# Kernel optimization log

Measured on AMD Instinct MI355X. Metric: run time of the kernel, lower is better.

Reference implementation:

```python
import jax, jax.numpy as jnp
import numpy as np

N_NODES = 100000
N_EDGES = 600000
DIM = 128


def mish(v):
    return v * jnp.tanh(jax.nn.softplus(v))


def setup_inputs() -> dict:
    key = jax.random.key(0)
    ks = jax.random.split(key, 10)
    x = jax.random.normal(ks[0], (N_NODES, DIM), dtype=jnp.float32)
    edge_attr = jax.random.normal(ks[1], (N_EDGES, DIM), dtype=jnp.float32)
    # build edges with src < dst guaranteed (so the torch mask edge_index[0]<edge_index[1] is all True)
    a = jax.random.randint(ks[2], (N_EDGES,), 0, N_NODES - 1)
    b = jax.random.randint(ks[3], (N_EDGES,), 0, N_NODES - 1)
    src = jnp.minimum(a, b)
    dst = jnp.maximum(a, b) + (src == jnp.maximum(a, b)).astype(a.dtype)  # fix ties, stays < N_NODES
    edge_index = jnp.stack([src, dst]).astype(jnp.int64)
    s1 = 1.0 / np.sqrt(2 * DIM)
    s2 = 1.0 / np.sqrt(DIM)
    eW1 = jax.random.uniform(ks[4], (2 * DIM, DIM), jnp.float32, -s1, s1)
    eW2 = jax.random.uniform(ks[5], (DIM, DIM), jnp.float32, -s2, s2)
    nW1 = jax.random.uniform(ks[6], (2 * DIM, DIM), jnp.float32, -s1, s1)
    nW2 = jax.random.uniform(ks[7], (DIM, DIM), jnp.float32, -s2, s2)
    zb = jnp.zeros((DIM,), jnp.float32)
    return {"x": x, "edge_attr": edge_attr, "edge_index": edge_index,
            "eW1": eW1, "eb1": zb, "eW2": eW2, "eb2": zb,
            "nW1": nW1, "nb1": zb, "nW2": nW2, "nb2": zb}


def reference(x, edge_attr, edge_index, eW1, eb1, eW2, eb2, nW1, nb1, nW2, nb2):
    src, dst = edge_index[0], edge_index[1]
    # mask src < dst is all-True by construction of edge_index (see setup_inputs)
    e_in = jnp.concatenate([edge_attr, x[src] + x[dst]], axis=-1)      # [E, 2d]
    e = mish(e_in @ eW1 + eb1) @ eW2 + eb2                             # [E, d]
    agg = jax.ops.segment_sum(edge_attr, dst, num_segments=N_NODES)    # scatter_sum over dst, padded to N
    x_in = jnp.concatenate([x, agg], axis=-1)                          # [N, 2d]
    x_out = mish(x_in @ nW1 + nb1) @ nW2 + nb2                         # [N, d]
    return x_out, e
```

## Files before the change

### kernel.cpp

```cpp
#include <hip/hip_runtime.h>

#define N_NODES 100000
#define N_EDGES 600000
#define DIM 128

#define AGG_BLOCKS  1024
#define EDGE_BLOCKS 2048

typedef __attribute__((ext_vector_type(8))) short short8;
typedef __attribute__((ext_vector_type(4))) float floatx4;
typedef unsigned short ushort_t;

#define MFMA(a,b,c) __builtin_amdgcn_mfma_f32_16x16x32_bf16((a),(b),(c),0,0,0)

__device__ __forceinline__ void bar_sync() {
    asm volatile("s_waitcnt lgkmcnt(0)" ::: "memory");
    __builtin_amdgcn_s_barrier();
    asm volatile("" ::: "memory");
}

__device__ __forceinline__ unsigned short f2bf(float f) {
    unsigned int u = __float_as_uint(f);
    u += 0x7fffu + ((u >> 16) & 1u);
    return (unsigned short)(u >> 16);
}

__device__ __forceinline__ short8 pack8(const float4& a, const float4& b) {
    short8 r;
    r[0] = (short)f2bf(a.x); r[1] = (short)f2bf(a.y);
    r[2] = (short)f2bf(a.z); r[3] = (short)f2bf(a.w);
    r[4] = (short)f2bf(b.x); r[5] = (short)f2bf(b.y);
    r[6] = (short)f2bf(b.z); r[7] = (short)f2bf(b.w);
    return r;
}

__device__ __forceinline__ short8 addpack_bf(short8 a, short8 b) {
    short8 r;
    #pragma unroll
    for (int i = 0; i < 8; ++i) {
        const float fa = __uint_as_float(((unsigned int)(unsigned short)a[i]) << 16);
        const float fb = __uint_as_float(((unsigned int)(unsigned short)b[i]) << 16);
        r[i] = (short)f2bf(fa + fb);
    }
    return r;
}

__device__ __forceinline__ float mish_f(float v) {
    if (v > 30.0f) return v;
    float t = __expf(v);
    float z = 1.0f + t;
    float z2 = z * z;
    return v * (z2 - 1.0f) / (z2 + 1.0f);
}

__device__ __forceinline__ short8 load_bfrag(const float* __restrict__ W,
                                             int ct, int kt, int lane) {
    const float* p = W + (size_t)(kt * 32 + (lane >> 4) * 8) * DIM + ct * 16 + (lane & 15);
    short8 r;
    #pragma unroll
    for (int j = 0; j < 8; ++j) r[j] = (short)f2bf(p[(size_t)j * DIM]);
    return r;
}

__device__ __forceinline__ void mlp_core(
    const ushort_t* __restrict__ s_in, ushort_t* __restrict__ s_h,
    const short8 (&w1f)[8], const short8 (&w2f)[4],
    float b1v, float b2v, float* __restrict__ out, int wave, int lane)
{
    const int r0 = lane & 15, q = lane >> 4, sw = lane & 7;

    floatx4 acc0 = {0.f,0.f,0.f,0.f}, acc1 = acc0;
    #pragma unroll
    for (int kt = 0; kt < 8; ++kt) {
        const int g = kt * 4 + q;
        short8 a0 = *(const short8*)&s_in[r0 * 256 + (g ^ sw) * 8];
        short8 a1 = *(const short8*)&s_in[(16 + r0) * 256 + (g ^ sw) * 8];
        acc0 = MFMA(a0, w1f[kt], acc0);
        acc1 = MFMA(a1, w1f[kt], acc1);
    }

    const int colg = wave * 2 + (r0 >> 3);
    const int bq   = r0 & 7;
    #pragma unroll
    for (int i = 0; i < 4; ++i) {
        int row = q * 4 + i;
        s_h[row * 128 + (colg ^ (row & 7)) * 8 + bq] = f2bf(mish_f(acc0[i] + b1v));
        row += 16;
        s_h[row * 128 + (colg ^ (row & 7)) * 8 + bq] = f2bf(mish_f(acc1[i] + b1v));
    }
    bar_sync();

    floatx4 c0 = {0.f,0.f,0.f,0.f}, c1 = c0;
    #pragma unroll
    for (int kt = 0; kt < 4; ++kt) {
        const int g = kt * 4 + q;
        short8 a0 = *(const short8*)&s_h[r0 * 128 + (g ^ sw) * 8];
        short8 a1 = *(const short8*)&s_h[(16 + r0) * 128 + (g ^ sw) * 8];
        c0 = MFMA(a0, w2f[kt], c0);
        c1 = MFMA(a1, w2f[kt], c1);
    }

    const int col = wave * 16 + r0;
    #pragma unroll
    for (int i = 0; i < 4; ++i) {
        __builtin_nontemporal_store(c0[i] + b2v, &out[(size_t)(q * 4 + i) * DIM + col]);
        __builtin_nontemporal_store(c1[i] + b2v, &out[(size_t)(16 + q * 4 + i) * DIM + col]);
    }
}


__global__ __launch_bounds__(256)
void zero_xbf_kernel(uint4* __restrict__ deg4, int n4,
                     const float* __restrict__ x, ushort_t* __restrict__ x_bf) {
    const int b = blockIdx.x;
    if (b < 98) {
        const int i = b * 256 + threadIdx.x;
        if (i < n4) deg4[i] = make_uint4(0u, 0u, 0u, 0u);
        return;
    }
    const int i = (b - 98) * 256 + threadIdx.x;
    const float* p = x + (size_t)i * 8;
    *(short8*)&x_bf[(size_t)i * 8] = pack8(*(const float4*)p, *(const float4*)(p + 4));
}

__global__ __launch_bounds__(256)
void hist_kernel(const int* __restrict__ dst_idx, int* __restrict__ deg) {
    const int e = blockIdx.x * 256 + threadIdx.x;
    if (e < N_EDGES) atomicAdd(&deg[dst_idx[e]], 1);
}

__global__ __launch_bounds__(1024)
void scan_a(const int* __restrict__ deg, int* __restrict__ tmp, int* __restrict__ partials) {
    __shared__ int sm[1024];
    const int t = threadIdx.x;
    const int i = blockIdx.x * 1024 + t;
    const int v = (i < N_NODES) ? deg[i] : 0;
    sm[t] = v; __syncthreads();
    for (int d = 1; d < 1024; d <<= 1) {
        int u = (t >= d) ? sm[t - d] : 0; __syncthreads();
        sm[t] += u; __syncthreads();
    }
    if (i < N_NODES) tmp[i] = sm[t] - v;
    if (t == 1023) partials[blockIdx.x] = sm[t];
}

__global__ __launch_bounds__(128)
void scan_b(const int* __restrict__ partials, int* __restrict__ poffs) {
    __shared__ int sm[128];
    const int t = threadIdx.x;
    const int v = (t < 98) ? partials[t] : 0;
    sm[t] = v; __syncthreads();
    for (int d = 1; d < 128; d <<= 1) {
        int u = (t >= d) ? sm[t - d] : 0; __syncthreads();
        sm[t] += u; __syncthreads();
    }
    poffs[t] = sm[t] - v;
}

__global__ __launch_bounds__(1024)
void scan_c(const int* __restrict__ tmp, const int* __restrict__ poffs,
            int* __restrict__ rowptr, int* __restrict__ cursor) {
    const int t = threadIdx.x;
    const int i = blockIdx.x * 1024 + t;
    if (i < N_NODES) {
        const int v = tmp[i] + poffs[blockIdx.x];
        rowptr[i] = v; cursor[i] = v;
    }
    if (i == 0) rowptr[N_NODES] = N_EDGES;
}

__global__ __launch_bounds__(256)
void scatter_kernel(const int* __restrict__ dst_idx, int* __restrict__ cursor,
                    int* __restrict__ perm) {
    const int e = blockIdx.x * 256 + threadIdx.x;
    if (e < N_EDGES) {
        const int pos = atomicAdd(&cursor[dst_idx[e]], 1);
        perm[pos] = e;
    }
}


__global__ __launch_bounds__(512)
void edge_agg_kernel(const ushort_t* __restrict__ x_bf,
                     const float* __restrict__ edge_attr,
                     const int* __restrict__ src_idx, const int* __restrict__ dst_idx,
                     const int* __restrict__ rowptr, const int* __restrict__ perm,
                     const float* __restrict__ W1, const float* __restrict__ b1,
                     const float* __restrict__ W2, const float* __restrict__ b2,
                     float* __restrict__ e_out, ushort_t* __restrict__ agg_bf)
{
    __shared__ ushort_t s_in[32 * 256];
    __shared__ ushort_t s_h[32 * 128];
    const int tid = threadIdx.x;

    if (blockIdx.x < AGG_BLOCKS) {
        const int sub = tid >> 4;
        const int ln  = tid & 15;
        for (int grp = blockIdx.x; grp < N_NODES / 32; grp += AGG_BLOCKS) {
            const int g = grp * 32 + sub;
            const int k0 = rowptr[g], k1 = rowptr[g + 1];
            float4 A0 = {0.f,0.f,0.f,0.f}, A1 = A0, B0 = A0, B1 = A0;
            int e0 = 0, e1 = 0, e2 = 0, e3 = 0;
            if (k0 < k1)     e0 = perm[k0];
            if (k0 + 1 < k1) e1 = perm[k0 + 1];
            if (k0 + 2 < k1) e2 = perm[k0 + 2];
            if (k0 + 3 < k1) e3 = perm[k0 + 3];
            int k = k0;
            for (; k + 3 < k1; k += 4) {
                const float* p0 = edge_attr + (size_t)e0 * DIM + ln * 8;
                const float* p1 = edge_attr + (size_t)e1 * DIM + ln * 8;
                const float* p2 = edge_attr + (size_t)e2 * DIM + ln * 8;
                const float* p3 = edge_attr + (size_t)e3 * DIM + ln * 8;
                const float4 a0 = *(const float4*)p0, a1 = *(const float4*)(p0 + 4);
                const float4 b0 = *(const float4*)p1, b1 = *(const float4*)(p1 + 4);
                const float4 c0 = *(const float4*)p2, c1 = *(const float4*)(p2 + 4);
                const float4 d0 = *(const float4*)p3, d1 = *(const float4*)(p3 + 4);
                if (k + 4 < k1) e0 = perm[k + 4];
                if (k + 5 < k1) e1 = perm[k + 5];
                if (k + 6 < k1) e2 = perm[k + 6];
                if (k + 7 < k1) e3 = perm[k + 7];
                A0.x += a0.x + c0.x; A0.y += a0.y + c0.y; A0.z += a0.z + c0.z; A0.w += a0.w + c0.w;
                A1.x += a1.x + c1.x; A1.y += a1.y + c1.y; A1.z += a1.z + c1.z; A1.w += a1.w + c1.w;
                B0.x += b0.x + d0.x; B0.y += b0.y + d0.y; B0.z += b0.z + d0.z; B0.w += b0.w + d0.w;
                B1.x += b1.x + d1.x; B1.y += b1.y + d1.y; B1.z += b1.z + d1.z; B1.w += b1.w + d1.w;
            }
            const int rem = k1 - k;
            if (rem > 0) {
                const float* p = edge_attr + (size_t)e0 * DIM + ln * 8;
                const float4 v0 = *(const float4*)p, v1 = *(const float4*)(p + 4);
                A0.x += v0.x; A0.y += v0.y; A0.z += v0.z; A0.w += v0.w;
                A1.x += v1.x; A1.y += v1.y; A1.z += v1.z; A1.w += v1.w;
            }
            if (rem > 1) {
                const float* p = edge_attr + (size_t)e1 * DIM + ln * 8;
                const float4 v0 = *(const float4*)p, v1 = *(const float4*)(p + 4);
                B0.x += v0.x; B0.y += v0.y; B0.z += v0.z; B0.w += v0.w;
                B1.x += v1.x; B1.y += v1.y; B1.z += v1.z; B1.w += v1.w;
            }
            if (rem > 2) {
                const float* p = edge_attr + (size_t)e2 * DIM + ln * 8;
                const float4 v0 = *(const float4*)p, v1 = *(const float4*)(p + 4);
                A0.x += v0.x; A0.y += v0.y; A0.z += v0.z; A0.w += v0.w;
                A1.x += v1.x; A1.y += v1.y; A1.z += v1.z; A1.w += v1.w;
            }
            A0.x += B0.x; A0.y += B0.y; A0.z += B0.z; A0.w += B0.w;
            A1.x += B1.x; A1.y += B1.y; A1.z += B1.z; A1.w += B1.w;
            *(short8*)&agg_bf[(size_t)g * DIM + ln * 8] = pack8(A0, A1);
        }
        return;
    }

    const int wave = tid >> 6, lane = tid & 63;

    short8 w1f[8], w2f[4];
    const float b1v = b1[wave * 16 + (lane & 15)];
    const float b2v = b2[wave * 16 + (lane & 15)];
    #pragma unroll
    for (int kt = 0; kt < 8; ++kt) w1f[kt] = load_bfrag(W1, wave, kt, lane);
    #pragma unroll
    for (int kt = 0; kt < 4; ++kt) w2f[kt] = load_bfrag(W2, wave, kt, lane);

    const int r = tid >> 4, gq = tid & 15, swr = r & 7;
    ushort_t* w_ea = &s_in[r * 256 + (gq ^ swr) * 8];
    ushort_t* w_x  = &s_in[r * 256 + ((16 + gq) ^ swr) * 8];

    const int ntiles = N_EDGES / 32;
    int t = blockIdx.x - AGG_BLOCKS;
    float4 ea0, ea1;
    short8 xsb, xdb;
    if (t < ntiles) {
        const int k = t * 32 + r;
        const int s = src_idx[k], d = dst_idx[k];
        const float* pe = edge_attr + (size_t)k * DIM + gq * 8;
        ea0 = *(const float4*)pe; ea1 = *(const float4*)(pe + 4);
        xsb = *(const short8*)&x_bf[(size_t)s * DIM + gq * 8];
        xdb = *(const short8*)&x_bf[(size_t)d * DIM + gq * 8];
    }
    for (; t < ntiles; t += EDGE_BLOCKS) {
        *(short8*)w_ea = pack8(ea0, ea1);
        *(short8*)w_x  = addpack_bf(xsb, xdb);

        const int tn = t + EDGE_BLOCKS;
        const bool more = tn < ntiles;
        int sN = 0, dN = 0;
        if (more) {
            const float* pe = edge_attr + (size_t)(tn * 32 + r) * DIM + gq * 8;
            ea0 = *(const float4*)pe; ea1 = *(const float4*)(pe + 4);
            const int k = tn * 32 + r;
            sN = src_idx[k]; dN = dst_idx[k];
        }
        bar_sync();
        if (more) {
            xsb = *(const short8*)&x_bf[(size_t)sN * DIM + gq * 8];
            xdb = *(const short8*)&x_bf[(size_t)dN * DIM + gq * 8];
        }
        mlp_core(s_in, s_h, w1f, w2f, b1v, b2v,
                 e_out + (size_t)t * 32 * DIM, wave, lane);
    }
}

__global__ __launch_bounds__(512)
void node_kernel(const float* __restrict__ x, const ushort_t* __restrict__ agg_bf,
                 const float* __restrict__ W1, const float* __restrict__ b1,
                 const float* __restrict__ W2, const float* __restrict__ b2,
                 float* __restrict__ x_out)
{
    __shared__ ushort_t s_in[32 * 256];
    __shared__ ushort_t s_h[32 * 128];
    const int tid = threadIdx.x, wave = tid >> 6, lane = tid & 63;

    short8 w1f[8], w2f[4];
    const float b1v = b1[wave * 16 + (lane & 15)];
    const float b2v = b2[wave * 16 + (lane & 15)];
    #pragma unroll
    for (int kt = 0; kt < 8; ++kt) w1f[kt] = load_bfrag(W1, wave, kt, lane);
    #pragma unroll
    for (int kt = 0; kt < 4; ++kt) w2f[kt] = load_bfrag(W2, wave, kt, lane);

    const int r = tid >> 4, gq = tid & 15, swr = r & 7;
    ushort_t* w_xp = &s_in[r * 256 + (gq ^ swr) * 8];
    ushort_t* w_ag = &s_in[r * 256 + ((16 + gq) ^ swr) * 8];

    const int ntiles = N_NODES / 32;
    int t = blockIdx.x;
    float4 xv0, xv1;
    short8 ag;
    if (t < ntiles) {
        const float* px = x + (size_t)(t * 32 + r) * DIM + gq * 8;
        xv0 = *(const float4*)px; xv1 = *(const float4*)(px + 4);
        ag  = *(const short8*)&agg_bf[(size_t)(t * 32 + r) * DIM + gq * 8];
    }
    for (; t < ntiles; t += gridDim.x) {
        *(short8*)w_xp = pack8(xv0, xv1);
        *(short8*)w_ag = ag;
        const int tn = t + gridDim.x;
        if (tn < ntiles) {
            const float* px = x + (size_t)(tn * 32 + r) * DIM + gq * 8;
            xv0 = *(const float4*)px; xv1 = *(const float4*)(px + 4);
            ag  = *(const short8*)&agg_bf[(size_t)(tn * 32 + r) * DIM + gq * 8];
        }
        bar_sync();
        mlp_core(s_in, s_h, w1f, w2f, b1v, b2v,
                 x_out + (size_t)t * 32 * DIM, wave, lane);
    }
}

extern "C" void kernel_launch(void* const* d_in, const int* in_sizes, int n_in,
                              void* d_out, int out_size, void* d_ws, size_t ws_size,
                              hipStream_t stream)
{
    const float* x         = (const float*)d_in[0];
    const float* edge_attr = (const float*)d_in[1];
    const int*   ei        = (const int*)d_in[2];
    const float* eW1 = (const float*)d_in[3];
    const float* eb1 = (const float*)d_in[4];
    const float* eW2 = (const float*)d_in[5];
    const float* eb2 = (const float*)d_in[6];
    const float* nW1 = (const float*)d_in[7];
    const float* nb1 = (const float*)d_in[8];
    const float* nW2 = (const float*)d_in[9];
    const float* nb2 = (const float*)d_in[10];

    float* out   = (float*)d_out;
    float* x_out = out;
    float* e_out = out + (size_t)N_NODES * DIM;

    const int* src_idx = ei;
    const int* dst_idx = ei + N_EDGES;

    int* wsi      = (int*)d_ws;
    int* deg      = wsi;
    int* tmp      = wsi + 100352;
    int* rowptr   = wsi + 200704;
    int* cursor   = wsi + 301056;
    int* perm     = wsi + 401408;
    int* partials = wsi + 1001408;
    int* poffs    = wsi + 1001536;
    ushort_t* agg_bf = (ushort_t*)(wsi + 1001664);

    ushort_t* x_bf = (ushort_t*)x_out;

    const int egrid = (N_EDGES + 255) / 256;
    zero_xbf_kernel<<<dim3(98 + 6250), dim3(256), 0, stream>>>(
        (uint4*)deg, 25088, x, x_bf);
    hist_kernel   <<<dim3(egrid), dim3(256),  0, stream>>>(dst_idx, deg);
    scan_a        <<<dim3(98),    dim3(1024), 0, stream>>>(deg, tmp, partials);
    scan_b        <<<dim3(1),     dim3(128),  0, stream>>>(partials, poffs);
    scan_c        <<<dim3(98),    dim3(1024), 0, stream>>>(tmp, poffs, rowptr, cursor);
    scatter_kernel<<<dim3(egrid), dim3(256),  0, stream>>>(dst_idx, cursor, perm);

    edge_agg_kernel<<<dim3(AGG_BLOCKS + EDGE_BLOCKS), dim3(512), 0, stream>>>(
        x_bf, edge_attr, src_idx, dst_idx, rowptr, perm,
        eW1, eb1, eW2, eb2, e_out, agg_bf);

    node_kernel<<<dim3(2048), dim3(512), 0, stream>>>(
        x, agg_bf, nW1, nb1, nW2, nb2, x_out);
}
```

Baseline: 367.2 us.

## Double-buffer LDS tiles to cut one barrier per MLP tile iteration

Splits the fused MLP into layer-1 and layer-2 phases and double-buffers the shared input and hidden tiles in both the edge and node kernels. The next tile's staging writes and the prefetch two tiles ahead now run between the two layers, so each iteration needs only one barrier instead of two. This doubles LDS use per block, which may lower occupancy, and drops the guard on the first tile load, which assumes every block has at least one tile.

```diff
diff --git a/kernel.cpp b/kernel.cpp
--- a/kernel.cpp
+++ b/kernel.cpp
@@ -62,44 +62,46 @@
     return r;
 }
 
-__device__ __forceinline__ void mlp_core(
-    const ushort_t* __restrict__ s_in, ushort_t* __restrict__ s_h,
-    const short8 (&w1f)[8], const short8 (&w2f)[4],
-    float b1v, float b2v, float* __restrict__ out, int wave, int lane)
+
+__device__ __forceinline__ void mlp_l1(
+    const ushort_t* __restrict__ s_in_p, ushort_t* __restrict__ s_h_p,
+    const short8 (&w1f)[8], float b1v, int wave, int lane)
 {
     const int r0 = lane & 15, q = lane >> 4, sw = lane & 7;
-
     floatx4 acc0 = {0.f,0.f,0.f,0.f}, acc1 = acc0;
     #pragma unroll
     for (int kt = 0; kt < 8; ++kt) {
         const int g = kt * 4 + q;
-        short8 a0 = *(const short8*)&s_in[r0 * 256 + (g ^ sw) * 8];
-        short8 a1 = *(const short8*)&s_in[(16 + r0) * 256 + (g ^ sw) * 8];
+        short8 a0 = *(const short8*)&s_in_p[r0 * 256 + (g ^ sw) * 8];
+        short8 a1 = *(const short8*)&s_in_p[(16 + r0) * 256 + (g ^ sw) * 8];
         acc0 = MFMA(a0, w1f[kt], acc0);
         acc1 = MFMA(a1, w1f[kt], acc1);
     }
-
     const int colg = wave * 2 + (r0 >> 3);
     const int bq   = r0 & 7;
     #pragma unroll
     for (int i = 0; i < 4; ++i) {
         int row = q * 4 + i;
-        s_h[row * 128 + (colg ^ (row & 7)) * 8 + bq] = f2bf(mish_f(acc0[i] + b1v));
+        s_h_p[row * 128 + (colg ^ (row & 7)) * 8 + bq] = f2bf(mish_f(acc0[i] + b1v));
         row += 16;
-        s_h[row * 128 + (colg ^ (row & 7)) * 8 + bq] = f2bf(mish_f(acc1[i] + b1v));
-    }
-    bar_sync();
-
+        s_h_p[row * 128 + (colg ^ (row & 7)) * 8 + bq] = f2bf(mish_f(acc1[i] + b1v));
+    }
+}
+
+__device__ __forceinline__ void mlp_l2(
+    const ushort_t* __restrict__ s_h_p,
+    const short8 (&w2f)[4], float b2v, float* __restrict__ out, int wave, int lane)
+{
+    const int r0 = lane & 15, q = lane >> 4, sw = lane & 7;
     floatx4 c0 = {0.f,0.f,0.f,0.f}, c1 = c0;
     #pragma unroll
     for (int kt = 0; kt < 4; ++kt) {
         const int g = kt * 4 + q;
-        short8 a0 = *(const short8*)&s_h[r0 * 128 + (g ^ sw) * 8];
-        short8 a1 = *(const short8*)&s_h[(16 + r0) * 128 + (g ^ sw) * 8];
+        short8 a0 = *(const short8*)&s_h_p[r0 * 128 + (g ^ sw) * 8];
+        short8 a1 = *(const short8*)&s_h_p[(16 + r0) * 128 + (g ^ sw) * 8];
         c0 = MFMA(a0, w2f[kt], c0);
         c1 = MFMA(a1, w2f[kt], c1);
     }
-
     const int col = wave * 16 + r0;
     #pragma unroll
     for (int i = 0; i < 4; ++i) {
@@ -189,8 +191,8 @@
                      const float* __restrict__ W2, const float* __restrict__ b2,
                      float* __restrict__ e_out, ushort_t* __restrict__ agg_bf)
 {
-    __shared__ ushort_t s_in[32 * 256];
-    __shared__ ushort_t s_h[32 * 128];
+    __shared__ ushort_t s_in[2][32 * 256];
+    __shared__ ushort_t s_h[2][32 * 128];
     const int tid = threadIdx.x;
 
     if (blockIdx.x < AGG_BLOCKS) {
@@ -261,14 +263,15 @@
     for (int kt = 0; kt < 4; ++kt) w2f[kt] = load_bfrag(W2, wave, kt, lane);
 
     const int r = tid >> 4, gq = tid & 15, swr = r & 7;
-    ushort_t* w_ea = &s_in[r * 256 + (gq ^ swr) * 8];
-    ushort_t* w_x  = &s_in[r * 256 + ((16 + gq) ^ swr) * 8];
+    const int woff_ea = r * 256 + (gq ^ swr) * 8;
+    const int woff_x  = r * 256 + ((16 + gq) ^ swr) * 8;
 
     const int ntiles = N_EDGES / 32;
     int t = blockIdx.x - AGG_BLOCKS;
+
     float4 ea0, ea1;
     short8 xsb, xdb;
-    if (t < ntiles) {
+    {
         const int k = t * 32 + r;
         const int s = src_idx[k], d = dst_idx[k];
         const float* pe = edge_attr + (size_t)k * DIM + gq * 8;
@@ -276,26 +279,41 @@
         xsb = *(const short8*)&x_bf[(size_t)s * DIM + gq * 8];
         xdb = *(const short8*)&x_bf[(size_t)d * DIM + gq * 8];
     }
-    for (; t < ntiles; t += EDGE_BLOCKS) {
-        *(short8*)w_ea = pack8(ea0, ea1);
-        *(short8*)w_x  = addpack_bf(xsb, xdb);
-
+    *(short8*)&s_in[0][woff_ea] = pack8(ea0, ea1);
+    *(short8*)&s_in[0][woff_x]  = addpack_bf(xsb, xdb);
+    {
         const int tn = t + EDGE_BLOCKS;
-        const bool more = tn < ntiles;
-        int sN = 0, dN = 0;
-        if (more) {
-            const float* pe = edge_attr + (size_t)(tn * 32 + r) * DIM + gq * 8;
+        if (tn < ntiles) {
+            const int k = tn * 32 + r;
+            const int s = src_idx[k], d = dst_idx[k];
+            const float* pe = edge_attr + (size_t)k * DIM + gq * 8;
             ea0 = *(const float4*)pe; ea1 = *(const float4*)(pe + 4);
-            const int k = tn * 32 + r;
-            sN = src_idx[k]; dN = dst_idx[k];
+            xsb = *(const short8*)&x_bf[(size_t)s * DIM + gq * 8];
+            xdb = *(const short8*)&x_bf[(size_t)d * DIM + gq * 8];
+        }
+    }
+    bar_sync();
+
+    int p = 0;
+    for (; t < ntiles; t += EDGE_BLOCKS, p ^= 1) {
+        mlp_l1(&s_in[p][0], &s_h[p][0], w1f, b1v, wave, lane);
+
+        const int tn = t + EDGE_BLOCKS;
+        if (tn < ntiles) {
+            *(short8*)&s_in[p ^ 1][woff_ea] = pack8(ea0, ea1);
+            *(short8*)&s_in[p ^ 1][woff_x]  = addpack_bf(xsb, xdb);
+            const int tnn = tn + EDGE_BLOCKS;
+            if (tnn < ntiles) {
+                const int k = tnn * 32 + r;
+                const int s = src_idx[k], d = dst_idx[k];
+                const float* pe = edge_attr + (size_t)k * DIM + gq * 8;
+                ea0 = *(const float4*)pe; ea1 = *(const float4*)(pe + 4);
+                xsb = *(const short8*)&x_bf[(size_t)s * DIM + gq * 8];
+                xdb = *(const short8*)&x_bf[(size_t)d * DIM + gq * 8];
+            }
         }
         bar_sync();
-        if (more) {
-            xsb = *(const short8*)&x_bf[(size_t)sN * DIM + gq * 8];
-            xdb = *(const short8*)&x_bf[(size_t)dN * DIM + gq * 8];
-        }
-        mlp_core(s_in, s_h, w1f, w2f, b1v, b2v,
-                 e_out + (size_t)t * 32 * DIM, wave, lane);
+        mlp_l2(&s_h[p][0], w2f, b2v, e_out + (size_t)t * 32 * DIM, wave, lane);
     }
 }
 
@@ -305,8 +323,8 @@
                  const float* __restrict__ W2, const float* __restrict__ b2,
                  float* __restrict__ x_out)
 {
-    __shared__ ushort_t s_in[32 * 256];
-    __shared__ ushort_t s_h[32 * 128];
+    __shared__ ushort_t s_in[2][32 * 256];
+    __shared__ ushort_t s_h[2][32 * 128];
     const int tid = threadIdx.x, wave = tid >> 6, lane = tid & 63;
 
     short8 w1f[8], w2f[4];
@@ -318,30 +336,48 @@
     for (int kt = 0; kt < 4; ++kt) w2f[kt] = load_bfrag(W2, wave, kt, lane);
 
     const int r = tid >> 4, gq = tid & 15, swr = r & 7;
-    ushort_t* w_xp = &s_in[r * 256 + (gq ^ swr) * 8];
-    ushort_t* w_ag = &s_in[r * 256 + ((16 + gq) ^ swr) * 8];
+    const int woff_x = r * 256 + (gq ^ swr) * 8;
+    const int woff_a = r * 256 + ((16 + gq) ^ swr) * 8;
 
     const int ntiles = N_NODES / 32;
     int t = blockIdx.x;
+
     float4 xv0, xv1;
     short8 ag;
-    if (t < ntiles) {
+    {
         const float* px = x + (size_t)(t * 32 + r) * DIM + gq * 8;
         xv0 = *(const float4*)px; xv1 = *(const float4*)(px + 4);
         ag  = *(const short8*)&agg_bf[(size_t)(t * 32 + r) * DIM + gq * 8];
     }
-    for (; t < ntiles; t += gridDim.x) {
-        *(short8*)w_xp = pack8(xv0, xv1);
-        *(short8*)w_ag = ag;
-        const int tn = t + gridDim.x;
+    *(short8*)&s_in[0][woff_x] = pack8(xv0, xv1);
+    *(short8*)&s_in[0][woff_a] = ag;
+    {
+        const int tn = t + (int)gridDim.x;
         if (tn < ntiles) {
             const float* px = x + (size_t)(tn * 32 + r) * DIM + gq * 8;
             xv0 = *(const float4*)px; xv1 = *(const float4*)(px + 4);
             ag  = *(const short8*)&agg_bf[(size_t)(tn * 32 + r) * DIM + gq * 8];
         }
+    }
+    bar_sync();
+
+    int p = 0;
+    const int G = gridDim.x;
+    for (; t < ntiles; t += G, p ^= 1) {
+        mlp_l1(&s_in[p][0], &s_h[p][0], w1f, b1v, wave, lane);
+        const int tn = t + G;
+        if (tn < ntiles) {
+            *(short8*)&s_in[p ^ 1][woff_x] = pack8(xv0, xv1);
+            *(short8*)&s_in[p ^ 1][woff_a] = ag;
+            const int tnn = tn + G;
+            if (tnn < ntiles) {
+                const float* px = x + (size_t)(tnn * 32 + r) * DIM + gq * 8;
+                xv0 = *(const float4*)px; xv1 = *(const float4*)(px + 4);
+                ag  = *(const short8*)&agg_bf[(size_t)(tnn * 32 + r) * DIM + gq * 8];
+            }
+        }
         bar_sync();
-        mlp_core(s_in, s_h, w1f, w2f, b1v, b2v,
-                 x_out + (size_t)t * 32 * DIM, wave, lane);
+        mlp_l2(&s_h[p][0], w2f, b2v, x_out + (size_t)t * 32 * DIM, wave, lane);
     }
 }
 
```

Result: slower. 446.8 us (+21.7%).
